# Kernel optimization log

Measured on AMD Instinct MI355X. Metric: run time of the kernel, lower is better.

## Reference

```python
import jax, jax.numpy as jnp
import numpy as np

N_EMBED = 384
N_HEAD = 6
HEAD_SIZE = N_EMBED // N_HEAD  # 64
LN_EPS = 1e-5


def setup_inputs() -> dict:
    key = jax.random.key(0)
    ks = jax.random.split(key, 12)
    B, T = 128, 256
    s_in = 1.0 / np.sqrt(N_EMBED)
    s_ff = 1.0 / np.sqrt(4 * N_EMBED)
    return {
        "x": jax.random.normal(ks[0], (B, T, N_EMBED), jnp.float32),
        "Wq": jax.random.normal(ks[1], (N_HEAD, N_EMBED, HEAD_SIZE), jnp.float32) * s_in,
        "Wk": jax.random.normal(ks[2], (N_HEAD, N_EMBED, HEAD_SIZE), jnp.float32) * s_in,
        "Wv": jax.random.normal(ks[3], (N_HEAD, N_EMBED, HEAD_SIZE), jnp.float32) * s_in,
        "Wproj": jax.random.normal(ks[4], (N_EMBED, N_EMBED), jnp.float32) * s_in,
        "bproj": jnp.zeros((N_EMBED,), jnp.float32),
        "W1": jax.random.normal(ks[5], (N_EMBED, 4 * N_EMBED), jnp.float32) * s_in,
        "b1": jnp.zeros((4 * N_EMBED,), jnp.float32),
        "W2": jax.random.normal(ks[6], (4 * N_EMBED, N_EMBED), jnp.float32) * s_ff,
        "b2": jnp.zeros((N_EMBED,), jnp.float32),
        "ln1_g": jnp.ones((N_EMBED,), jnp.float32),
        "ln1_b": jnp.zeros((N_EMBED,), jnp.float32),
        "ln2_g": jnp.ones((N_EMBED,), jnp.float32),
        "ln2_b": jnp.zeros((N_EMBED,), jnp.float32),
    }


def _layernorm(x, g, b):
    mu = jnp.mean(x, axis=-1, keepdims=True)
    var = jnp.mean(jnp.square(x - mu), axis=-1, keepdims=True)
    return (x - mu) * jax.lax.rsqrt(var + LN_EPS) * g + b


def _attention(xn, Wq, Wk, Wv, Wproj, bproj):
    B, T, C = xn.shape
    q = jnp.einsum("btc,hcd->bhtd", xn, Wq)
    k = jnp.einsum("btc,hcd->bhtd", xn, Wk)
    v = jnp.einsum("btc,hcd->bhtd", xn, Wv)
    # NOTE: original scales by C**-0.5 with C = n_embed (384), not head_size
    scores = jnp.einsum("bhtd,bhsd->bhts", q, k) * (C ** -0.5)
    causal = jnp.tril(jnp.ones((T, T), bool))
    scores = jnp.where(causal, scores, -jnp.inf)
    wei = jax.nn.softmax(scores, axis=-1)
    out = jnp.einsum("bhts,bhsd->bhtd", wei, v)
    out = out.transpose(0, 2, 1, 3).reshape(B, T, N_EMBED)  # concat heads
    return out @ Wproj + bproj


def reference(x, Wq, Wk, Wv, Wproj, bproj, W1, b1, W2, b2, ln1_g, ln1_b, ln2_g, ln2_b):
    x = x + _attention(_layernorm(x, ln1_g, ln1_b), Wq, Wk, Wv, Wproj, bproj)
    h = _layernorm(x, ln2_g, ln2_b)
    ff = jax.nn.relu(h @ W1 + b1) @ W2 + b2
    return x + ff
```

## Files before the change

### kernel.cpp

```cpp
#include <hip/hip_runtime.h>
#include <hip/hip_bf16.h>

typedef __hip_bfloat16 bf16;
typedef __attribute__((ext_vector_type(8))) short bf16x8;
typedef __attribute__((ext_vector_type(4))) float f32x4;

#define CEMB 384
#define NHEAD 6
#define HSZ 64
#define TSEQ 256
#define BATCH 128
#define MROWS (BATCH*TSEQ)
#define FDIM 1536
#define QSCALE 0.05103103630798288f
#define SMAX 8.0f

#define AS1 __attribute__((address_space(1)))
#define AS3 __attribute__((address_space(3)))
__device__ __forceinline__ void gload16(const void* g, void* l){
  __builtin_amdgcn_global_load_lds((const AS1 unsigned*)(g), (AS3 unsigned*)(l), 16, 0, 0);
}
__device__ __forceinline__ float b2f(unsigned short u){
  unsigned int xi = ((unsigned int)u)<<16; float f; __builtin_memcpy(&f,&xi,4); return f;
}

__global__ __launch_bounds__(256) void ln_kernel(const float* __restrict__ x,
    const float* __restrict__ gam, const float* __restrict__ bet,
    bf16* __restrict__ y)
{
  const int row  = blockIdx.x*4 + (threadIdx.x>>6);
  const int lane = threadIdx.x & 63;
  const float* xr = x + (size_t)row*CEMB;
  float v[6]; float s = 0.f;
  #pragma unroll
  for (int i=0;i<6;i++){ v[i] = xr[lane + i*64]; s += v[i]; }
  #pragma unroll
  for (int m=1;m<64;m<<=1) s += __shfl_xor(s, m, 64);
  const float mu = s * (1.0f/CEMB);
  float qs = 0.f;
  #pragma unroll
  for (int i=0;i<6;i++){ v[i] -= mu; qs += v[i]*v[i]; }
  #pragma unroll
  for (int m=1;m<64;m<<=1) qs += __shfl_xor(qs, m, 64);
  const float rs = rsqrtf(qs*(1.0f/CEMB) + 1e-5f);
  bf16* yr = y + (size_t)row*CEMB;
  #pragma unroll
  for (int i=0;i<6;i++){
    int c = lane + i*64;
    yr[c] = __float2bfloat16(v[i]*rs*gam[c] + bet[c]);
  }
}

__global__ __launch_bounds__(256) void ln_kernel_b(const bf16* __restrict__ x,
    const float* __restrict__ gam, const float* __restrict__ bet,
    bf16* __restrict__ y)
{
  const int row  = blockIdx.x*4 + (threadIdx.x>>6);
  const int lane = threadIdx.x & 63;
  const ushort2* xr = (const ushort2*)(x + (size_t)row*CEMB);
  float v[6]; float s = 0.f;
  #pragma unroll
  for (int i=0;i<3;i++){
    ushort2 u = xr[lane + i*64];
    v[2*i]   = b2f(u.x); v[2*i+1] = b2f(u.y);
    s += v[2*i] + v[2*i+1];
  }
  #pragma unroll
  for (int m=1;m<64;m<<=1) s += __shfl_xor(s, m, 64);
  const float mu = s * (1.0f/CEMB);
  float qs = 0.f;
  #pragma unroll
  for (int i=0;i<6;i++){ v[i] -= mu; qs += v[i]*v[i]; }
  #pragma unroll
  for (int m=1;m<64;m<<=1) qs += __shfl_xor(qs, m, 64);
  const float rs = rsqrtf(qs*(1.0f/CEMB) + 1e-5f);
  bf16* yr = y + (size_t)row*CEMB;
  #pragma unroll
  for (int i=0;i<3;i++)
    #pragma unroll
    for (int j=0;j<2;j++){
      int c = (lane + i*64)*2 + j;
      yr[c] = __float2bfloat16(v[2*i+j]*rs*gam[c] + bet[c]);
    }
}

__global__ __launch_bounds__(256) void transpose_to_bf16(const float* __restrict__ src,
    bf16* __restrict__ dst, int K, int N)
{
  __shared__ float tile[32][33];
  const int n0 = blockIdx.x*32, k0 = blockIdx.y*32;
  src += (size_t)blockIdx.z*K*N;
  dst += (size_t)blockIdx.z*K*N;
  const int c = threadIdx.x & 31, r8 = threadIdx.x >> 5;
  #pragma unroll
  for (int i=0;i<4;i++)
    tile[r8 + i*8][c] = src[(size_t)(k0 + r8 + i*8)*N + n0 + c];
  __syncthreads();
  #pragma unroll
  for (int i=0;i<4;i++)
    dst[(size_t)(n0 + r8 + i*8)*K + k0 + c] = __float2bfloat16(tile[c][r8 + i*8]);
}

__global__ __launch_bounds__(256) void transpose_qkv(const float* __restrict__ Wq,
    const float* __restrict__ Wk, const float* __restrict__ Wv, bf16* __restrict__ dst)
{
  __shared__ float tile[32][33];
  const int z = blockIdx.z;
  const float* src = (z < 6) ? Wq : (z < 12 ? Wk : Wv);
  src += (size_t)(z % 6) * CEMB * HSZ;
  dst += (size_t)z * CEMB * HSZ;
  const int n0 = blockIdx.x*32, k0 = blockIdx.y*32;
  const int c = threadIdx.x & 31, r8 = threadIdx.x >> 5;
  #pragma unroll
  for (int i=0;i<4;i++)
    tile[r8 + i*8][c] = src[(size_t)(k0 + r8 + i*8)*HSZ + n0 + c];
  __syncthreads();
  #pragma unroll
  for (int i=0;i<4;i++)
    dst[(size_t)(n0 + r8 + i*8)*CEMB + k0 + c] = __float2bfloat16(tile[c][r8 + i*8]);
}

template<int EPI, int NN, int NK>
__global__ __launch_bounds__(512) void gemm2(
    const bf16* __restrict__ A, const bf16* __restrict__ BT,
    const float* __restrict__ bias, const float* __restrict__ resid,
    float* __restrict__ outf, bf16* __restrict__ outb0,
    bf16* __restrict__ outb1, bf16* __restrict__ outb2)
{
  constexpr int K = NK*32;
  constexpr int N = NN*128;
  __shared__ char lA[2][256*64];
  __shared__ char lB[2][128*64];
  const int cpx = gridDim.x >> 3;
  const int wg  = (blockIdx.x & 7)*cpx + (blockIdx.x >> 3);
  const int bm = (wg / NN)*256, bn = (wg % NN)*128;
  const int t = threadIdx.x, lane = t & 63, wid = t >> 6;
  const int wr = (wid>>1)*64, wc = (wid&1)*64;
  const int g = lane >> 4, fr = lane & 15;
  const size_t rowK2 = (size_t)K*2;
  f32x4 acc[4][4] = {};

  auto stage = [&](int buf, int kt){
    const size_t ko = (size_t)kt*64;
    #pragma unroll
    for (int i=0;i<2;i++){
      int slot = t + i*512;
      int row = slot>>2, blk = slot&3;
      gload16((const char*)A + (size_t)(bm+row)*rowK2 + ko + ((blk ^ ((row>>1)&3))<<4),
              lA[buf] + slot*16);
    }
    {
      int row = t>>2, blk = t&3;
      gload16((const char*)BT + (size_t)(bn+row)*rowK2 + ko + ((blk ^ ((row>>1)&3))<<4),
              lB[buf] + t*16);
    }
  };

  stage(0, 0);
  __syncthreads();
  int cur = 0;
  #pragma unroll 1
  for (int kt=0; kt<NK; ++kt){
    if (kt+1 < NK) stage(cur^1, kt+1);
    bf16x8 af[4], bq[4];
    #pragma unroll
    for (int mi=0;mi<4;mi++){
      int row = wr + mi*16 + fr;
      af[mi] = *(const bf16x8*)(lA[cur] + row*64 + ((g ^ ((row>>1)&3))<<4));
    }
    #pragma unroll
    for (int nj=0;nj<4;nj++){
      int row = wc + nj*16 + fr;
      bq[nj] = *(const bf16x8*)(lB[cur] + row*64 + ((g ^ ((row>>1)&3))<<4));
    }
    __builtin_amdgcn_s_setprio(1);
    #pragma unroll
    for (int mi=0;mi<4;mi++)
      #pragma unroll
      for (int nj=0;nj<4;nj++)
        acc[mi][nj] = __builtin_amdgcn_mfma_f32_16x16x32_bf16(af[mi], bq[nj], acc[mi][nj], 0, 0, 0);
    __builtin_amdgcn_s_setprio(0);
    __syncthreads();
    cur ^= 1;
  }

  if constexpr (EPI==0){
    const int sel = bn/CEMB;
    bf16* dst = sel==0 ? outb0 : (sel==1 ? outb1 : outb2);
    const float sc = sel==0 ? QSCALE : 1.0f;
    const int nb = bn - sel*CEMB;
    #pragma unroll
    for (int nj=0;nj<4;nj++){
      const int nn = nb + wc + nj*16 + fr;
      const int hh = nn>>6, dd = nn&63;
      #pragma unroll
      for (int mi=0;mi<4;mi++){
        const int m0 = bm + wr + mi*16 + 4*g;
        const int bb = m0>>8, tt0 = m0&255;
        bf16* p = dst + ((size_t)(bb*NHEAD + hh)*TSEQ + tt0)*HSZ + dd;
        #pragma unroll
        for (int e=0;e<4;e++)
          p[(size_t)e*HSZ] = __float2bfloat16(acc[mi][nj][e]*sc);
      }
    }
  } else {
    #pragma unroll
    for (int mi=0;mi<4;mi++)
      #pragma unroll
      for (int nj=0;nj<4;nj++)
        #pragma unroll
        for (int e=0;e<4;e++){
          const int m = bm + wr + mi*16 + 4*g + e;
          const int n = bn + wc + nj*16 + fr;
          const float vacc = acc[mi][nj][e];
          if constexpr (EPI==1){
            outb0[(size_t)m*N + n] = __float2bfloat16(vacc + bias[n] + resid[(size_t)m*N + n]);
          } else {
            float z = vacc + bias[n];
            outb0[(size_t)m*N + n] = __float2bfloat16(z > 0.f ? z : 0.f);
          }
        }
  }
}

template<int NK>
__global__ __launch_bounds__(512, 2) void gemm8n(
    const bf16* __restrict__ A, const bf16* __restrict__ BT,
    const float* __restrict__ bias, const bf16* __restrict__ residb,
    float* __restrict__ outf)
{
  constexpr int K = NK*64;
  __shared__ char lds[114688];
  const int cpx = gridDim.x >> 3;
  const int wg  = (blockIdx.x & 7)*cpx + (blockIdx.x >> 3);
  const int bm = (wg >> 1)*256, bn = (wg & 1)*192;
  const int t = threadIdx.x, lane = t & 63, wid = t >> 6;
  const int wm = wid >> 2, wn = wid & 3;
  const int g = lane >> 4, fr = lane & 15;
  const size_t rowb = (size_t)K*2;
  const int sblkA = ((t&3) ^ ((t>>3)&3)) << 4;
  const int swzA  = (g ^ ((fr>>1)&3)) << 4;
  f32x4 acc[8][3] = {};

  const char* Ag = (const char*)A + (size_t)(bm + (t>>2))*rowb + sblkA;
  const size_t rstep = rowb*128;

  auto stgA = [&](int KH, int sl, int kt2){
    const char* src = Ag + (size_t)kt2*128 + KH*64;
    char* dst = lds + sl*32768 + KH*16384 + wid*1024;
    gload16(src,         dst);
    gload16(src + rstep, dst + 8192);
  };
  auto stgB = [&](int sl, int kt2){
    #pragma unroll
    for (int j=0;j<3;j++){
      int slot = t + j*512;
      int row = slot>>3, blk = slot&7;
      gload16((const char*)BT + (size_t)(bn + row)*rowb + (size_t)kt2*128 + ((blk ^ (row&7))<<4),
              lds + 65536 + sl*24576 + j*8192 + wid*1024);
    }
  };
  auto rdA = [&](bf16x8* af, int sl, int MH, int KS){
    const char* p = lds + sl*32768 + KS*16384 + (wm*128 + MH*64 + fr)*64 + swzA;
    #pragma unroll
    for (int mi=0;mi<4;mi++) af[mi] = *(const bf16x8*)(p + mi*1024);
  };
  auto rdB = [&](bf16x8* bq, int sl, int ks){
    #pragma unroll
    for (int nj=0;nj<3;nj++){
      int row = wn*48 + nj*16 + fr;
      bq[nj] = *(const bf16x8*)(lds + 65536 + sl*24576 + row*128 + (((ks*4+g) ^ (row&7))<<4));
    }
  };

#define MFMA12(MH) \
  __builtin_amdgcn_s_setprio(1); \
  _Pragma("unroll") \
  for (int mi=0;mi<4;mi++){ \
    _Pragma("unroll") \
    for (int nj=0;nj<3;nj++) \
      acc[(MH)*4+mi][nj] = __builtin_amdgcn_mfma_f32_16x16x32_bf16(af[mi], bq[nj], acc[(MH)*4+mi][nj], 0, 0, 0); \
  } \
  __builtin_amdgcn_s_setprio(0);

  stgA(0,0,0); stgB(0,0); stgA(1,0,0);
  asm volatile("s_waitcnt vmcnt(2)" ::: "memory");
  __builtin_amdgcn_s_barrier();

  #pragma unroll 1
  for (int kt=0; kt<NK; ++kt){
    const int sl = kt&1, sn = sl^1;
    const bool pf = (kt+1 < NK);
    bf16x8 af[4], bq[3];
    rdA(af, sl, 0, 0); rdB(bq, sl, 0);
    if (pf) stgA(0,sn,kt+1);
    __builtin_amdgcn_s_barrier();
    asm volatile("s_waitcnt lgkmcnt(0)" ::: "memory");
    __builtin_amdgcn_sched_barrier(0);
    MFMA12(0)
    __builtin_amdgcn_s_barrier();
    rdA(af, sl, 1, 0);
    if (pf){ stgB(sn,kt+1);
             asm volatile("s_waitcnt vmcnt(5)" ::: "memory"); }
    else     asm volatile("s_waitcnt vmcnt(0)" ::: "memory");
    __builtin_amdgcn_s_barrier();
    asm volatile("s_waitcnt lgkmcnt(0)" ::: "memory");
    __builtin_amdgcn_sched_barrier(0);
    MFMA12(1)
    __builtin_amdgcn_s_barrier();
    rdA(af, sl, 0, 1); rdB(bq, sl, 1);
    if (pf) stgA(1,sn,kt+1);
    __builtin_amdgcn_s_barrier();
    asm volatile("s_waitcnt lgkmcnt(0)" ::: "memory");
    __builtin_amdgcn_sched_barrier(0);
    MFMA12(0)
    __builtin_amdgcn_s_barrier();
    rdA(af, sl, 1, 1);
    if (pf) asm volatile("s_waitcnt vmcnt(2)" ::: "memory");
    __builtin_amdgcn_s_barrier();
    asm volatile("s_waitcnt lgkmcnt(0)" ::: "memory");
    __builtin_amdgcn_sched_barrier(0);
    MFMA12(1)
    __builtin_amdgcn_s_barrier();
  }
#undef MFMA12

  #pragma unroll
  for (int mi=0;mi<8;mi++)
    #pragma unroll
    for (int nj=0;nj<3;nj++)
      #pragma unroll
      for (int e=0;e<4;e++){
        const int m = bm + wm*128 + mi*16 + 4*g + e;
        const int n = bn + wn*48 + nj*16 + fr;
        outf[(size_t)m*CEMB + n] = acc[mi][nj][e] + bias[n] +
            b2f(*(const unsigned short*)&residb[(size_t)m*CEMB + n]);
      }
}

__global__ __launch_bounds__(256) void attn_kernel(
    const bf16* __restrict__ q, const bf16* __restrict__ k,
    const bf16* __restrict__ v, bf16* __restrict__ out)
{
  __shared__ char kt_lds[64*128];
  __shared__ char vt_lds[80*128];
  __shared__ char p_lds[4][64*128];
  const int bh = blockIdx.x;
  const int bidx = bh / NHEAD, hidx = bh - bidx*NHEAD;
  const int t = threadIdx.x, lane = t & 63, w = t >> 6;
  const int g = lane >> 4, fr = lane & 15;
  const int lrow = lane >> 3;
  const int scol = ((lane & 7) ^ lrow) << 4;
  const size_t base = (size_t)bh * TSEQ * HSZ;

  if (t < 128){
    unsigned int ones2 = 0x3F803F80u;
    uint4 vv;
    if ((t>>3) == 0) vv = uint4{ones2, ones2, ones2, ones2};
    else             vv = uint4{0u, 0u, 0u, 0u};
    *(uint4*)(vt_lds + (64 + (t>>3))*128 + (t&7)*16) = vv;
  }

  bf16x8 qf[4][2];
  #pragma unroll
  for (int mi=0;mi<4;mi++)
    #pragma unroll
    for (int ks=0;ks<2;ks++)
      qf[mi][ks] = *(const bf16x8*)(q + base + (size_t)(w*64 + mi*16 + fr)*HSZ + ks*32 + g*8);

  f32x4 of[4][5] = {};

  for (int j=0;j<4;j++){
    __syncthreads();
    #pragma unroll
    for (int i=0;i<2;i++){
      int r0 = w*16 + i*8;
      gload16((const char*)(k + base + (size_t)(j*64 + r0 + lrow)*HSZ) + scol,
              kt_lds + r0*128);
    }
    #pragma unroll
    for (int i=0;i<2;i++){
      int chunk = t + i*256, r = chunk>>3, c = chunk&7;
      uint4 vv = *(const uint4*)(v + base + (size_t)(j*64 + r)*HSZ + c*8);
      const unsigned short* pv = (const unsigned short*)&vv;
      #pragma unroll
      for (int u=0;u<8;u++)
        *(unsigned short*)(vt_lds + (c*8+u)*128 + ((((r>>3) ^ u ^ c)&7)<<4) + (r&7)*2) = pv[u];
    }
    __syncthreads();
    if (j <= w){
      f32x4 sa[4][4] = {};
      #pragma unroll
      for (int ks=0;ks<2;ks++){
        bf16x8 kf[4];
        #pragma unroll
        for (int nj=0;nj<4;nj++)
          kf[nj] = *(const bf16x8*)(kt_lds + (nj*16+fr)*128 + (((ks*4+g)*16) ^ ((fr&7)<<4)));
        __builtin_amdgcn_s_setprio(1);
        #pragma unroll
        for (int mi=0;mi<4;mi++)
          #pragma unroll
          for (int nj=0;nj<4;nj++)
            sa[mi][nj] = __builtin_amdgcn_mfma_f32_16x16x32_bf16(qf[mi][ks], kf[nj], sa[mi][nj], 0, 0, 0);
        __builtin_amdgcn_s_setprio(0);
      }
      if (j == w){
        #pragma unroll
        for (int mi=0;mi<4;mi++)
          #pragma unroll
          for (int nj=0;nj<4;nj++)
            #pragma unroll
            for (int e=0;e<4;e++)
              if (nj*16 + fr > mi*16 + 4*g + e) sa[mi][nj][e] = -1e30f;
      }
      char* pl = p_lds[w];
      #pragma unroll
      for (int mi=0;mi<4;mi++)
        #pragma unroll
        for (int nj=0;nj<4;nj++)
          #pragma unroll
          for (int e=0;e<4;e++){
            int row = mi*16 + 4*g + e, col = nj*16 + fr;
            float p = __expf(sa[mi][nj][e] - SMAX);
            *(bf16*)(pl + row*128 + (((col>>3) ^ (row&7))<<4) + (col&7)*2) =
                __float2bfloat16(p);
          }
      #pragma unroll
      for (int ks=0;ks<2;ks++){
        bf16x8 pa[4], vf[5];
        #pragma unroll
        for (int mi=0;mi<4;mi++)
          pa[mi] = *(const bf16x8*)(pl + (mi*16+fr)*128 + (((ks*4+g)*16) ^ ((fr&7)<<4)));
        #pragma unroll
        for (int nd=0;nd<5;nd++){
          int d = nd*16 + fr;
          vf[nd] = *(const bf16x8*)(vt_lds + d*128 +
                   ((((ks*4+g) ^ (d&7) ^ ((d>>3)&7))&7)<<4));
        }
        __builtin_amdgcn_s_setprio(1);
        #pragma unroll
        for (int mi=0;mi<4;mi++)
          #pragma unroll
          for (int nd=0;nd<5;nd++)
            of[mi][nd] = __builtin_amdgcn_mfma_f32_16x16x32_bf16(pa[mi], vf[nd], of[mi][nd], 0, 0, 0);
        __builtin_amdgcn_s_setprio(0);
      }
    }
  }
  #pragma unroll
  for (int mi=0;mi<4;mi++){
    float rl[4];
    #pragma unroll
    for (int e=0;e<4;e++){
      float l = __shfl(of[mi][4][e], (int)(lane & 48), 64);
      rl[e] = 1.0f / l;
    }
    #pragma unroll
    for (int nd=0;nd<4;nd++)
      #pragma unroll
      for (int e=0;e<4;e++){
        int row = w*64 + mi*16 + 4*g + e;
        int d = nd*16 + fr;
        out[(size_t)(bidx*TSEQ + row)*CEMB + hidx*HSZ + d] =
            __float2bfloat16(of[mi][nd][e] * rl[e]);
      }
  }
}

extern "C" void kernel_launch(void* const* d_in, const int* in_sizes, int n_in,
                              void* d_out, int out_size, void* d_ws, size_t ws_size,
                              hipStream_t stream)
{
  const float* x     = (const float*)d_in[0];
  const float* Wq    = (const float*)d_in[1];
  const float* Wk    = (const float*)d_in[2];
  const float* Wv    = (const float*)d_in[3];
  const float* Wproj = (const float*)d_in[4];
  const float* bproj = (const float*)d_in[5];
  const float* W1    = (const float*)d_in[6];
  const float* b1    = (const float*)d_in[7];
  const float* W2    = (const float*)d_in[8];
  const float* b2    = (const float*)d_in[9];
  const float* ln1g  = (const float*)d_in[10];
  const float* ln1b  = (const float*)d_in[11];
  const float* ln2g  = (const float*)d_in[12];
  const float* ln2b  = (const float*)d_in[13];

  char* ws = (char*)d_ws;
  const size_t SA = (size_t)MROWS*CEMB*2;
  bf16* xn1    = (bf16*)(ws + 0*SA);
  bf16* qb     = (bf16*)(ws + 1*SA);
  bf16* kbuf   = (bf16*)(ws + 2*SA);
  bf16* vb     = (bf16*)(ws + 3*SA);
  bf16* attn_o = (bf16*)(ws + 0*SA);
  bf16* act    = (bf16*)(ws + 0*SA);
  bf16* hb     = (bf16*)(ws + 4*SA);
  bf16* x1b    = (bf16*)(ws + 5*SA);
  char* wb     = ws + 5*SA + (size_t)MROWS*CEMB*4;
  bf16* qkvT   = (bf16*)wb;
  bf16* projT  = (bf16*)(wb + (size_t)1152*384*2);
  bf16* w1T    = (bf16*)(wb + (size_t)(1152+384)*384*2);
  bf16* w2T    = (bf16*)(wb + (size_t)(1152+384+1536)*384*2);

  dim3 blk(256), blk5(512);
  transpose_qkv<<<dim3(2,12,18), blk, 0, stream>>>(Wq, Wk, Wv, qkvT);
  transpose_to_bf16<<<dim3(12,12,1), blk, 0, stream>>>(Wproj, projT, CEMB, CEMB);
  transpose_to_bf16<<<dim3(48,12,1), blk, 0, stream>>>(W1,    w1T,   CEMB, FDIM);
  transpose_to_bf16<<<dim3(12,48,1), blk, 0, stream>>>(W2,    w2T,   FDIM, CEMB);

  ln_kernel<<<dim3(MROWS/4), blk, 0, stream>>>(x, ln1g, ln1b, xn1);
  gemm2<0,9,12><<<dim3(1152), blk5, 0, stream>>>(xn1, qkvT, nullptr, nullptr,
                                                 nullptr, qb, kbuf, vb);
  attn_kernel<<<dim3(768), blk, 0, stream>>>(qb, kbuf, vb, attn_o);
  gemm2<1,3,12><<<dim3(384), blk5, 0, stream>>>(attn_o, projT, bproj, x,
                                                nullptr, x1b, nullptr, nullptr);
  ln_kernel_b<<<dim3(MROWS/4), blk, 0, stream>>>(x1b, ln2g, ln2b, hb);
  gemm2<2,12,12><<<dim3(1536), blk5, 0, stream>>>(hb, w1T, b1, nullptr,
                                                  nullptr, act, nullptr, nullptr);
  gemm8n<24><<<dim3(256), blk5, 0, stream>>>(act, w2T, b2, x1b, (float*)d_out);
}
```

Before: 250.9 us.

## Triple-buffer GEMM LDS staging with explicit vmcnt waits

```diff
diff --git a/kernel.cpp b/kernel.cpp
--- a/kernel.cpp
+++ b/kernel.cpp
@@ -121,7 +121,7 @@
 }
 
 template<int EPI, int NN, int NK>
-__global__ __launch_bounds__(512) void gemm2(
+__global__ __launch_bounds__(512) void gemm5(
     const bf16* __restrict__ A, const bf16* __restrict__ BT,
     const float* __restrict__ bias, const float* __restrict__ resid,
     float* __restrict__ outf, bf16* __restrict__ outb0,
@@ -129,8 +129,8 @@
 {
   constexpr int K = NK*32;
   constexpr int N = NN*128;
-  __shared__ char lA[2][256*64];
-  __shared__ char lB[2][128*64];
+  __shared__ char lA[3][256*64];
+  __shared__ char lB[3][128*64];
   const int cpx = gridDim.x >> 3;
   const int wg  = (blockIdx.x & 7)*cpx + (blockIdx.x >> 3);
   const int bm = (wg / NN)*256, bn = (wg % NN)*128;
@@ -140,28 +140,31 @@
   const size_t rowK2 = (size_t)K*2;
   f32x4 acc[4][4] = {};
 
-  auto stage = [&](int buf, int kt){
+  auto stage = [&](int sl, int kt){
     const size_t ko = (size_t)kt*64;
     #pragma unroll
     for (int i=0;i<2;i++){
       int slot = t + i*512;
       int row = slot>>2, blk = slot&3;
       gload16((const char*)A + (size_t)(bm+row)*rowK2 + ko + ((blk ^ ((row>>1)&3))<<4),
-              lA[buf] + slot*16);
+              lA[sl] + slot*16);
     }
     {
       int row = t>>2, blk = t&3;
       gload16((const char*)BT + (size_t)(bn+row)*rowK2 + ko + ((blk ^ ((row>>1)&3))<<4),
-              lB[buf] + t*16);
+              lB[sl] + t*16);
     }
   };
 
-  stage(0, 0);
-  __syncthreads();
-  int cur = 0;
+  stage(0,0); stage(1,1); stage(2,2);
   #pragma unroll 1
   for (int kt=0; kt<NK; ++kt){
-    if (kt+1 < NK) stage(cur^1, kt+1);
+    const int rem = NK-1-kt;
+    if (rem >= 2)      asm volatile("s_waitcnt vmcnt(6)" ::: "memory");
+    else if (rem == 1) asm volatile("s_waitcnt vmcnt(3)" ::: "memory");
+    else               asm volatile("s_waitcnt vmcnt(0)" ::: "memory");
+    __builtin_amdgcn_s_barrier();
+    const int cur = kt%3;
     bf16x8 af[4], bq[4];
     #pragma unroll
     for (int mi=0;mi<4;mi++){
@@ -173,6 +176,10 @@
       int row = wc + nj*16 + fr;
       bq[nj] = *(const bf16x8*)(lB[cur] + row*64 + ((g ^ ((row>>1)&3))<<4));
     }
+    asm volatile("s_waitcnt lgkmcnt(0)" ::: "memory");
+    __builtin_amdgcn_sched_barrier(0);
+    __builtin_amdgcn_s_barrier();
+    if (kt+3 < NK) stage(cur, kt+3);
     __builtin_amdgcn_s_setprio(1);
     #pragma unroll
     for (int mi=0;mi<4;mi++)
@@ -180,8 +187,6 @@
       for (int nj=0;nj<4;nj++)
         acc[mi][nj] = __builtin_amdgcn_mfma_f32_16x16x32_bf16(af[mi], bq[nj], acc[mi][nj], 0, 0, 0);
     __builtin_amdgcn_s_setprio(0);
-    __syncthreads();
-    cur ^= 1;
   }
 
   if constexpr (EPI==0){
@@ -509,13 +514,13 @@
   transpose_to_bf16<<<dim3(12,48,1), blk, 0, stream>>>(W2,    w2T,   FDIM, CEMB);
 
   ln_kernel<<<dim3(MROWS/4), blk, 0, stream>>>(x, ln1g, ln1b, xn1);
-  gemm2<0,9,12><<<dim3(1152), blk5, 0, stream>>>(xn1, qkvT, nullptr, nullptr,
+  gemm5<0,9,12><<<dim3(1152), blk5, 0, stream>>>(xn1, qkvT, nullptr, nullptr,
                                                  nullptr, qb, kbuf, vb);
   attn_kernel<<<dim3(768), blk, 0, stream>>>(qb, kbuf, vb, attn_o);
-  gemm2<1,3,12><<<dim3(384), blk5, 0, stream>>>(attn_o, projT, bproj, x,
+  gemm5<1,3,12><<<dim3(384), blk5, 0, stream>>>(attn_o, projT, bproj, x,
                                                 nullptr, x1b, nullptr, nullptr);
   ln_kernel_b<<<dim3(MROWS/4), blk, 0, stream>>>(x1b, ln2g, ln2b, hb);
-  gemm2<2,12,12><<<dim3(1536), blk5, 0, stream>>>(hb, w1T, b1, nullptr,
+  gemm5<2,12,12><<<dim3(1536), blk5, 0, stream>>>(hb, w1T, b1, nullptr,
                                                   nullptr, act, nullptr, nullptr);
   gemm8n<24><<<dim3(256), blk5, 0, stream>>>(act, w2T, b2, x1b, (float*)d_out);
 }
```

After: 248.4 us. No clear change (-1.0%).
